# Performance work log

Measured on AMD Instinct MI355X. Metric: run time of the kernel, lower is better.

Reference implementation:

```python
import jax, jax.numpy as jnp
import numpy as np

B, N, D = 2, 2048, 1024
H, ENC = 16, 8
HD = D // H
EPS = 1e-5


def _apply_rope(x, cos, sin):
    # x: [B,N,H,HD], cos/sin: [N,HD//2]
    c = cos[None, :, None, :]
    s = sin[None, :, None, :]
    x_re = x[..., 0::2]
    x_im = x[..., 1::2]
    out = jnp.stack([x_re * c - x_im * s, x_re * s + x_im * c], axis=-1)
    return out.reshape(x.shape)


def _rmsnorm(x):
    return x * jax.lax.rsqrt(jnp.mean(x * x, axis=-1, keepdims=True) + EPS)


def setup_inputs() -> dict:
    key = jax.random.key(0)
    ks = jax.random.split(key, 8)
    pos = jnp.arange(N, dtype=jnp.float32)[:, None]
    inv_freq = 1.0 / (10000.0 ** (jnp.arange(0, HD, 2, dtype=jnp.float32) / HD))  # [HD//2]
    ang = pos * inv_freq[None, :]
    std = 0.02
    return {
        "x": jax.random.normal(ks[0], (B, N, D), dtype=jnp.float32),
        "rope_cos": jnp.cos(ang),
        "rope_sin": jnp.sin(ang),
        "Wq": std * jax.random.normal(ks[1], (D, D), dtype=jnp.float32),
        "Wk": std * jax.random.normal(ks[2], (D, D), dtype=jnp.float32),
        "Wv": std * jax.random.normal(ks[3], (D, D), dtype=jnp.float32),
        "Wo_enc": std * jax.random.normal(ks[4], (H * HD, D), dtype=jnp.float32),
        "Wo_dec": std * jax.random.normal(ks[5], ((H - ENC) * HD, D), dtype=jnp.float32),
        "heads": H,
        "encoder_heads": ENC,
    }


def reference(x, rope_cos, rope_sin, Wq, Wk, Wv, Wo_enc, Wo_dec, heads, encoder_heads):
    b, n, d = x.shape
    hd = d // heads
    scale = hd ** (-0.5)
    q = (x @ Wq).reshape(b, n, heads, hd)
    k = (x @ Wk).reshape(b, n, heads, hd)
    v = (x @ Wv).reshape(b, n, heads, hd)
    q = _rmsnorm(_apply_rope(q, rope_cos, rope_sin))
    k = _rmsnorm(_apply_rope(k, rope_cos, rope_sin))
    # scores: [B,H,N,N]
    scores = jnp.einsum("bihd,bjhd->bhij", q, k) * scale
    causal = jnp.tril(jnp.ones((n, n), dtype=bool))  # [N,N]
    is_enc = (jnp.arange(heads) < encoder_heads)[:, None, None]  # [H,1,1]
    allow = jnp.logical_or(is_enc, causal[None, :, :])  # [H,N,N]
    scores = jnp.where(allow[None], scores, -jnp.inf)
    att = jax.nn.softmax(scores, axis=-1)
    out = jnp.einsum("bhij,bjhd->bihd", att, v)  # [B,N,H,HD]
    enc_out = out.reshape(b, n, heads * hd) @ Wo_enc
    dec_out = out[:, :, encoder_heads:, :].reshape(b, n, (heads - encoder_heads) * hd) @ Wo_dec
    return (enc_out, dec_out)
```

## Files before the change

### kernel.cpp

```cpp
#include <hip/hip_runtime.h>
#include <hip/hip_bf16.h>
#include <math.h>

#define B_    2
#define N_    2048
#define D_    1024
#define H_    16
#define ENC_  8
#define HD_   64
#define EPS_  1e-5f
#define M_    (B_ * N_)

typedef __bf16 bf16x8 __attribute__((ext_vector_type(8)));
typedef __bf16 bf16x2 __attribute__((ext_vector_type(2)));
typedef float  f32x4  __attribute__((ext_vector_type(4)));

#define MB(x) ((size_t)(x) * 1024 * 1024)

#define KSC_  0.18033688011112042f

#if __has_builtin(__builtin_amdgcn_exp2f)
#define EXP2F(x) __builtin_amdgcn_exp2f(x)
#else
#define EXP2F(x) exp2f(x)
#endif

__device__ __forceinline__ void gld16(const __bf16* g, __bf16* l) {
    __builtin_amdgcn_global_load_lds(
        (const __attribute__((address_space(1))) void*)g,
        (__attribute__((address_space(3))) void*)l,
        16, 0, 0);
}

template <typename OutT>
__device__ __forceinline__ void gemm_core(
    const __bf16* __restrict__ A, const __bf16* __restrict__ Bt,
    OutT* __restrict__ C, int K, int lda, int aoff, int ldc,
    int bm, int bn, __bf16* As, __bf16* Bs)
{
    const int tid  = threadIdx.x;
    const int w    = tid >> 6;
    const int lane = tid & 63;
    const int lrow = lane & 15;
    const int quad = lane >> 4;
    const int wr   = w >> 1;
    const int wc   = w & 1;

    const int sr = lane >> 2;
    const int sc = (lane & 3) * 8;
    const __bf16* Ag0 = A  + (size_t)(bm +      w * 16 + sr) * lda + aoff + sc;
    const __bf16* Ag1 = A  + (size_t)(bm + 64 + w * 16 + sr) * lda + aoff + sc;
    const __bf16* Bg0 = Bt + (size_t)(bn +      w * 16 + sr) * K + sc;
    const __bf16* Bg1 = Bt + (size_t)(bn + 64 + w * 16 + sr) * K + sc;
    __bf16* Al0 = &As[w * 512];
    __bf16* Al1 = &As[2048 + w * 512];
    __bf16* Bl0 = &Bs[w * 512];
    __bf16* Bl1 = &Bs[2048 + w * 512];

    f32x4 acc[4][4];
    #pragma unroll
    for (int i = 0; i < 4; ++i)
        #pragma unroll
        for (int j = 0; j < 4; ++j) acc[i][j] = (f32x4){0.f, 0.f, 0.f, 0.f};

    for (int k0 = 0; k0 < K; k0 += 32) {
        gld16(Ag0 + k0, Al0);
        gld16(Ag1 + k0, Al1);
        gld16(Bg0 + k0, Bl0);
        gld16(Bg1 + k0, Bl1);
        __syncthreads();

        bf16x8 af[4], bf[4];
        #pragma unroll
        for (int rt = 0; rt < 4; ++rt)
            af[rt] = *(const bf16x8*)&As[(wr * 64 + rt * 16 + lrow) * 32 + quad * 8];
        #pragma unroll
        for (int ct = 0; ct < 4; ++ct)
            bf[ct] = *(const bf16x8*)&Bs[(wc * 64 + ct * 16 + lrow) * 32 + quad * 8];

        #pragma unroll
        for (int rt = 0; rt < 4; ++rt)
            #pragma unroll
            for (int ct = 0; ct < 4; ++ct)
                acc[rt][ct] = __builtin_amdgcn_mfma_f32_16x16x32_bf16(
                    af[rt], bf[ct], acc[rt][ct], 0, 0, 0);
        __syncthreads();
    }

    #pragma unroll
    for (int rt = 0; rt < 4; ++rt)
        #pragma unroll
        for (int ct = 0; ct < 4; ++ct)
            #pragma unroll
            for (int r = 0; r < 4; ++r) {
                const int row = bm + wr * 64 + rt * 16 + quad * 4 + r;
                const int col = bn + wc * 64 + ct * 16 + lrow;
                C[(size_t)row * ldc + col] = (OutT)acc[rt][ct][r];
            }
}

__global__ __launch_bounds__(256) void gemm_qkv(
    const __bf16* __restrict__ A, const __bf16* __restrict__ Bt,
    __bf16* __restrict__ C)
{
    __shared__ __bf16 As[128 * 32];
    __shared__ __bf16 Bs[128 * 32];
    gemm_core<__bf16>(A, Bt, C, D_, D_, 0, 3072,
                      blockIdx.y * 128, blockIdx.x * 128, As, Bs);
}

__global__ __launch_bounds__(256) void gemm_out(
    const __bf16* __restrict__ A, const __bf16* __restrict__ Woe,
    const __bf16* __restrict__ Wod, float* __restrict__ Cenc,
    float* __restrict__ Cdec)
{
    __shared__ __bf16 As[128 * 32];
    __shared__ __bf16 Bs[128 * 32];
    const int bx = blockIdx.x;
    if (bx < 8) {
        gemm_core<float>(A, Woe, Cenc, 1024, D_, 0, D_,
                         blockIdx.y * 128, bx * 128, As, Bs);
    } else {
        gemm_core<float>(A, Wod, Cdec, 512, D_, 512, D_,
                         blockIdx.y * 128, (bx - 8) * 128, As, Bs);
    }
}

struct WtArgs {
    const float* W[5];
    __bf16*      Wt[5];
    int          K[5];
    int          nyb[5];
    const float* x;
    __bf16*      xbf;
};

__global__ __launch_bounds__(256) void wt_conv_all(WtArgs ar)
{
    const int z = blockIdx.z;
    if (z >= 5) {
        const int linear = (z - 5) * 256 + blockIdx.y * 16 + blockIdx.x;
        const size_t i = ((size_t)linear * 256 + threadIdx.x) * 8;
        float4 a = *(const float4*)&ar.x[i];
        float4 b = *(const float4*)&ar.x[i + 4];
        bf16x8 o = {(__bf16)a.x, (__bf16)a.y, (__bf16)a.z, (__bf16)a.w,
                    (__bf16)b.x, (__bf16)b.y, (__bf16)b.z, (__bf16)b.w};
        *(bf16x8*)&ar.xbf[i] = o;
        return;
    }
    if (blockIdx.y >= ar.nyb[z]) return;
    const float* W  = ar.W[z];
    __bf16*      Wt = ar.Wt[z];
    const int    K  = ar.K[z];

    __shared__ __bf16 t[64][72];
    const int kb = blockIdx.y * 64;
    const int nb = blockIdx.x * 64;
    {
        const int kl = threadIdx.x >> 2;
        const int c0 = (threadIdx.x & 3) * 16;
        const float* src = W + (size_t)(kb + kl) * D_ + nb + c0;
        #pragma unroll
        for (int u = 0; u < 4; ++u) {
            float4 f = *(const float4*)&src[u * 4];
            t[c0 + u * 4 + 0][kl] = (__bf16)f.x;
            t[c0 + u * 4 + 1][kl] = (__bf16)f.y;
            t[c0 + u * 4 + 2][kl] = (__bf16)f.z;
            t[c0 + u * 4 + 3][kl] = (__bf16)f.w;
        }
    }
    __syncthreads();
    {
        const int nl  = threadIdx.x >> 2;
        const int k0c = (threadIdx.x & 3) * 16;
        __bf16* dst = Wt + (size_t)(nb + nl) * K + kb + k0c;
        *(bf16x8*)&dst[0] = *(const bf16x8*)&t[nl][k0c];
        *(bf16x8*)&dst[8] = *(const bf16x8*)&t[nl][k0c + 8];
    }
}

__global__ __launch_bounds__(256) void rope_vconv(
    const __bf16* __restrict__ qkv,
    const float* __restrict__ cs, const float* __restrict__ sn,
    __bf16* __restrict__ qbf, __bf16* __restrict__ kbf,
    __bf16* __restrict__ vt)
{
    if (blockIdx.x < 16384) {
        const int row  = blockIdx.x * 4 + (threadIdx.x >> 6);
        const int lane = threadIdx.x & 63;
        const int n    = (row >> 4) & (N_ - 1);
        const int b    = row >> 15;
        const int h    = row & 15;
        const int p    = lane >> 1;

        const float c = cs[n * (HD_ / 2) + p];
        const float s = sn[n * (HD_ / 2) + p];
        const size_t ibase = (size_t)(b * N_ + n) * 3072 + h * HD_ + lane;
        const size_t obase = ((size_t)(b * H_ + h) * N_ + n) * HD_ + lane;
        const bool odd = (lane & 1);

        {
            float val = (float)qkv[ibase];
            float partner = __shfl_xor(val, 1, 64);
            float r = odd ? fmaf(partner, s, val * c)
                          : (val * c - partner * s);
            float ss = r * r;
            #pragma unroll
            for (int off = 1; off < 64; off <<= 1) ss += __shfl_xor(ss, off, 64);
            qbf[obase] = (__bf16)(r * rsqrtf(ss * (1.0f / 64.0f) + EPS_) * KSC_);
        }
        {
            float val = (float)qkv[ibase + 1024];
            float partner = __shfl_xor(val, 1, 64);
            float r = odd ? fmaf(partner, s, val * c)
                          : (val * c - partner * s);
            float ss = r * r;
            #pragma unroll
            for (int off = 1; off < 64; off <<= 1) ss += __shfl_xor(ss, off, 64);
            kbf[obase] = (__bf16)(r * rsqrtf(ss * (1.0f / 64.0f) + EPS_));
        }
    } else {
        __shared__ __bf16 tile[64][72];
        const int bx = blockIdx.x - 16384;
        const int bh = bx >> 5;
        const int b  = bh >> 4, h = bh & 15;
        const int n0 = (bx & 31) * 64;
        {
            const int nl = threadIdx.x >> 2;
            const int d0 = (threadIdx.x & 3) * 16;
            const __bf16* src =
                qkv + (size_t)(b * N_ + n0 + nl) * 3072 + 2048 + h * HD_ + d0;
            bf16x8 v0 = *(const bf16x8*)&src[0];
            bf16x8 v1 = *(const bf16x8*)&src[8];
            #pragma unroll
            for (int e = 0; e < 8; ++e) {
                tile[d0 + e][nl]     = v0[e];
                tile[d0 + 8 + e][nl] = v1[e];
            }
        }
        __syncthreads();
        {
            const int dl = threadIdx.x >> 2;
            const int nc = (threadIdx.x & 3) * 16;
            __bf16* dst = vt + ((size_t)(bh * HD_ + dl)) * N_ + n0 + nc;
            bf16x8 o0, o1;
            #pragma unroll
            for (int e = 0; e < 8; ++e) {
                const int p0 = nc + e;
                const int p1 = nc + 8 + e;
                o0[e] = tile[dl][(p0 & ~31) + (((p0 >> 2) & 1) << 4)
                                 + (((p0 >> 3) & 3) << 2) + (p0 & 3)];
                o1[e] = tile[dl][(p1 & ~31) + (((p1 >> 2) & 1) << 4)
                                 + (((p1 >> 3) & 3) << 2) + (p1 & 3)];
            }
            *(bf16x8*)&dst[0] = o0;
            *(bf16x8*)&dst[8] = o1;
        }
    }
}

template <int NG, bool DEC>
__device__ __forceinline__ void attn_core(
    const __bf16* __restrict__ qbase, const __bf16* __restrict__ kbase,
    const __bf16* __restrict__ vbase, __bf16* __restrict__ o,
    int b, int h, int qb, int ntiles,
    __bf16 (*Ks)[4096], __bf16 (*Vs)[4096])
{
    const int tid  = threadIdx.x;
    const int w    = tid >> 6;
    const int lane = tid & 63;
    const int lrow = lane & 15;
    const int quad = lane >> 4;

    const __bf16* kg0 = kbase + (size_t)lane * HD_ + w * 8;
    const __bf16* kg1 = kbase + (size_t)lane * HD_ + (w + 4) * 8;
    const __bf16* vg  = vbase + (size_t)lane * N_;

    int i0g[NG];
    #pragma unroll
    for (int g = 0; g < NG; ++g) i0g[g] = qb * (NG * 64) + g * 64 + w * 16;

    bf16x8 qf[NG][2];
    #pragma unroll
    for (int g = 0; g < NG; ++g)
        #pragma unroll
        for (int kc = 0; kc < 2; ++kc)
            qf[g][kc] = *(const bf16x8*)
                &qbase[(size_t)(i0g[g] + lrow) * HD_ + kc * 32 + quad * 8];

    const f32x4 zero = {0.f, 0.f, 0.f, 0.f};
    f32x4 oacc[NG][4];
    float lsum[NG];
    #pragma unroll
    for (int g = 0; g < NG; ++g) {
        lsum[g] = 0.f;
        #pragma unroll
        for (int c = 0; c < 4; ++c) oacc[g][c] = zero;
    }

    auto stage = [&](int t, int bb) {
        const int j0 = t << 6;
        gld16(kg0 + (size_t)j0 * HD_, &Ks[bb][(w)     * 512]);
        gld16(kg1 + (size_t)j0 * HD_, &Ks[bb][(w + 4) * 512]);
        gld16(vg + j0 + w * 8,        &Vs[bb][(w)     * 512]);
        gld16(vg + j0 + (w + 4) * 8,  &Vs[bb][(w + 4) * 512]);
    };

    stage(0, 0);
    for (int t = 0; t < ntiles; ++t) {
        const int bb = t & 1;
        __syncthreads();
        if (t + 1 < ntiles) stage(t + 1, bb ^ 1);

        const int j64 = t << 6;
        const bool do1 = !DEC || (j64 + 32 <= i0g[0] + 15);

        bf16x8 pf[2][NG];

        {
            bf16x8 kf0 = *(const bf16x8*)&Ks[bb][((quad)     * 64 + lrow) * 8];
            bf16x8 kf1 = *(const bf16x8*)&Ks[bb][((4 + quad) * 64 + lrow) * 8];
            bf16x8 kf2 = *(const bf16x8*)&Ks[bb][((quad)     * 64 + 16 + lrow) * 8];
            bf16x8 kf3 = *(const bf16x8*)&Ks[bb][((4 + quad) * 64 + 16 + lrow) * 8];

            f32x4 s0[NG], s1[NG];
            #pragma unroll
            for (int g = 0; g < NG; ++g) { s0[g] = zero; s1[g] = zero; }
            #pragma unroll
            for (int g = 0; g < NG; ++g)
                s0[g] = __builtin_amdgcn_mfma_f32_16x16x32_bf16(kf0, qf[g][0], s0[g], 0, 0, 0);
            #pragma unroll
            for (int g = 0; g < NG; ++g)
                s0[g] = __builtin_amdgcn_mfma_f32_16x16x32_bf16(kf1, qf[g][1], s0[g], 0, 0, 0);
            #pragma unroll
            for (int g = 0; g < NG; ++g)
                s1[g] = __builtin_amdgcn_mfma_f32_16x16x32_bf16(kf2, qf[g][0], s1[g], 0, 0, 0);
            #pragma unroll
            for (int g = 0; g < NG; ++g)
                s1[g] = __builtin_amdgcn_mfma_f32_16x16x32_bf16(kf3, qf[g][1], s1[g], 0, 0, 0);

            #pragma unroll
            for (int g = 0; g < NG; ++g) {
                float pA[4], pB[4];
                if (DEC && (j64 + 31 > i0g[g])) {
                    const int i = i0g[g] + lrow;
                    #pragma unroll
                    for (int r = 0; r < 4; ++r) {
                        const int k0 = j64 + quad * 4 + r;
                        pA[r] = (k0      <= i) ? EXP2F(s0[g][r]) : 0.f;
                        pB[r] = (k0 + 16 <= i) ? EXP2F(s1[g][r]) : 0.f;
                    }
                } else {
                    #pragma unroll
                    for (int r = 0; r < 4; ++r) {
                        pA[r] = EXP2F(s0[g][r]);
                        pB[r] = EXP2F(s1[g][r]);
                    }
                }
                lsum[g] += (pA[0] + pA[1]) + (pA[2] + pA[3])
                         + (pB[0] + pB[1]) + (pB[2] + pB[3]);
                pf[0][g] = (bf16x8){(__bf16)pA[0], (__bf16)pA[1],
                                    (__bf16)pA[2], (__bf16)pA[3],
                                    (__bf16)pB[0], (__bf16)pB[1],
                                    (__bf16)pB[2], (__bf16)pB[3]};
            }
        }

        if (do1) {
            bf16x8 kf0 = *(const bf16x8*)&Ks[bb][((quad)     * 64 + 32 + lrow) * 8];
            bf16x8 kf1 = *(const bf16x8*)&Ks[bb][((4 + quad) * 64 + 32 + lrow) * 8];
            bf16x8 kf2 = *(const bf16x8*)&Ks[bb][((quad)     * 64 + 48 + lrow) * 8];
            bf16x8 kf3 = *(const bf16x8*)&Ks[bb][((4 + quad) * 64 + 48 + lrow) * 8];

            f32x4 s0[NG], s1[NG];
            #pragma unroll
            for (int g = 0; g < NG; ++g) { s0[g] = zero; s1[g] = zero; }
            #pragma unroll
            for (int g = 0; g < NG; ++g)
                s0[g] = __builtin_amdgcn_mfma_f32_16x16x32_bf16(kf0, qf[g][0], s0[g], 0, 0, 0);
            #pragma unroll
            for (int g = 0; g < NG; ++g)
                s0[g] = __builtin_amdgcn_mfma_f32_16x16x32_bf16(kf1, qf[g][1], s0[g], 0, 0, 0);
            #pragma unroll
            for (int g = 0; g < NG; ++g)
                s1[g] = __builtin_amdgcn_mfma_f32_16x16x32_bf16(kf2, qf[g][0], s1[g], 0, 0, 0);
            #pragma unroll
            for (int g = 0; g < NG; ++g)
                s1[g] = __builtin_amdgcn_mfma_f32_16x16x32_bf16(kf3, qf[g][1], s1[g], 0, 0, 0);

            const int jp = j64 + 32;
            #pragma unroll
            for (int g = 0; g < NG; ++g) {
                float pA[4], pB[4];
                if (DEC && (jp + 31 > i0g[g])) {
                    const int i = i0g[g] + lrow;
                    #pragma unroll
                    for (int r = 0; r < 4; ++r) {
                        const int k0 = jp + quad * 4 + r;
                        pA[r] = (k0      <= i) ? EXP2F(s0[g][r]) : 0.f;
                        pB[r] = (k0 + 16 <= i) ? EXP2F(s1[g][r]) : 0.f;
                    }
                } else {
                    #pragma unroll
                    for (int r = 0; r < 4; ++r) {
                        pA[r] = EXP2F(s0[g][r]);
                        pB[r] = EXP2F(s1[g][r]);
                    }
                }
                lsum[g] += (pA[0] + pA[1]) + (pA[2] + pA[3])
                         + (pB[0] + pB[1]) + (pB[2] + pB[3]);
                pf[1][g] = (bf16x8){(__bf16)pA[0], (__bf16)pA[1],
                                    (__bf16)pA[2], (__bf16)pA[3],
                                    (__bf16)pB[0], (__bf16)pB[1],
                                    (__bf16)pB[2], (__bf16)pB[3]};
            }
        }

        {
            bf16x8 vf0 = *(const bf16x8*)&Vs[bb][((quad) * 64 +  0 + lrow) * 8];
            bf16x8 vf1 = *(const bf16x8*)&Vs[bb][((quad) * 64 + 16 + lrow) * 8];
            bf16x8 vf2 = *(const bf16x8*)&Vs[bb][((quad) * 64 + 32 + lrow) * 8];
            bf16x8 vf3 = *(const bf16x8*)&Vs[bb][((quad) * 64 + 48 + lrow) * 8];
            #pragma unroll
            for (int g = 0; g < NG; ++g) {
                oacc[g][0] = __builtin_amdgcn_mfma_f32_16x16x32_bf16(pf[0][g], vf0, oacc[g][0], 0, 0, 0);
                oacc[g][1] = __builtin_amdgcn_mfma_f32_16x16x32_bf16(pf[0][g], vf1, oacc[g][1], 0, 0, 0);
                oacc[g][2] = __builtin_amdgcn_mfma_f32_16x16x32_bf16(pf[0][g], vf2, oacc[g][2], 0, 0, 0);
                oacc[g][3] = __builtin_amdgcn_mfma_f32_16x16x32_bf16(pf[0][g], vf3, oacc[g][3], 0, 0, 0);
            }
        }

        if (do1) {
            bf16x8 vf0 = *(const bf16x8*)&Vs[bb][((4 + quad) * 64 +  0 + lrow) * 8];
            bf16x8 vf1 = *(const bf16x8*)&Vs[bb][((4 + quad) * 64 + 16 + lrow) * 8];
            bf16x8 vf2 = *(const bf16x8*)&Vs[bb][((4 + quad) * 64 + 32 + lrow) * 8];
            bf16x8 vf3 = *(const bf16x8*)&Vs[bb][((4 + quad) * 64 + 48 + lrow) * 8];
            #pragma unroll
            for (int g = 0; g < NG; ++g) {
                oacc[g][0] = __builtin_amdgcn_mfma_f32_16x16x32_bf16(pf[1][g], vf0, oacc[g][0], 0, 0, 0);
                oacc[g][1] = __builtin_amdgcn_mfma_f32_16x16x32_bf16(pf[1][g], vf1, oacc[g][1], 0, 0, 0);
                oacc[g][2] = __builtin_amdgcn_mfma_f32_16x16x32_bf16(pf[1][g], vf2, oacc[g][2], 0, 0, 0);
                oacc[g][3] = __builtin_amdgcn_mfma_f32_16x16x32_bf16(pf[1][g], vf3, oacc[g][3], 0, 0, 0);
            }
        }
    }

    float lrec[NG][4];
    #pragma unroll
    for (int g = 0; g < NG; ++g) {
        float s = lsum[g];
        s += __shfl_xor(s, 16, 64);
        s += __shfl_xor(s, 32, 64);
        s = 1.0f / s;
        #pragma unroll
        for (int r = 0; r < 4; ++r)
            lrec[g][r] = __shfl(s, quad * 4 + r, 64);
    }

    #pragma unroll
    for (int g = 0; g < NG; ++g)
        #pragma unroll
        for (int c = 0; c < 4; ++c)
            #pragma unroll
            for (int r = 0; r < 4; ++r) {
                const int i = i0g[g] + quad * 4 + r;
                o[(size_t)(b * N_ + i) * D_ + h * HD_ + c * 16 + lrow] =
                    (__bf16)(oacc[g][c][r] * lrec[g][r]);
            }
}

__global__ __launch_bounds__(256) void attn_mfma(
    const __bf16* __restrict__ qbf, const __bf16* __restrict__ kbf,
    const __bf16* __restrict__ vtbf, __bf16* __restrict__ o)
{
    __shared__ __bf16 Ks[2][4096];
    __shared__ __bf16 Vs[2][4096];

    if (blockIdx.x < 256) {
        const int e  = blockIdx.x & 15;
        const int bh = (e >> 3) * 16 + (e & 7);
        const int qb = blockIdx.x >> 4;
        attn_core<2, false>(
            qbf  + (size_t)bh * N_ * HD_, kbf + (size_t)bh * N_ * HD_,
            vtbf + (size_t)bh * HD_ * N_, o,
            bh >> 4, bh & 15, qb, N_ >> 6, Ks, Vs);
    } else {
        const int idx = blockIdx.x - 256;
        const int d   = idx & 15;
        const int bh  = (d >> 3) * 16 + 8 + (d & 7);
        const int p   = idx >> 4;
        const int qb  = (p < 16) ? (31 - p) : (p - 16);
        attn_core<1, true>(
            qbf  + (size_t)bh * N_ * HD_, kbf + (size_t)bh * N_ * HD_,
            vtbf + (size_t)bh * HD_ * N_, o,
            bh >> 4, bh & 15, qb, qb + 1, Ks, Vs);
    }
}

extern "C" void kernel_launch(void* const* d_in, const int* in_sizes, int n_in,
                              void* d_out, int out_size, void* d_ws, size_t ws_size,
                              hipStream_t stream)
{
    const float* x   = (const float*)d_in[0];
    const float* cs  = (const float*)d_in[1];
    const float* sn  = (const float*)d_in[2];
    const float* Wq  = (const float*)d_in[3];
    const float* Wk  = (const float*)d_in[4];
    const float* Wv  = (const float*)d_in[5];
    const float* Woe = (const float*)d_in[6];
    const float* Wod = (const float*)d_in[7];

    float* enc_out = (float*)d_out;
    float* dec_out = enc_out + (size_t)M_ * D_;

    char* ws = (char*)d_ws;
    __bf16* xbf    = (__bf16*)(ws);
    __bf16* wqkv_t = (__bf16*)(ws + MB(8));
    __bf16* woe_t  = (__bf16*)(ws + MB(14));
    __bf16* wod_t  = (__bf16*)(ws + MB(16));
    __bf16* qkv    = (__bf16*)(ws + MB(17));
    __bf16* qbf    = (__bf16*)(ws + MB(41));
    __bf16* kbf    = (__bf16*)(ws + MB(49));
    __bf16* vtbf   = xbf;
    __bf16* obuf   = qkv;

    WtArgs wa;
    wa.W[0] = Wq;  wa.Wt[0] = wqkv_t;                 wa.K[0] = 1024; wa.nyb[0] = 16;
    wa.W[1] = Wk;  wa.Wt[1] = wqkv_t + 1024 * 1024;   wa.K[1] = 1024; wa.nyb[1] = 16;
    wa.W[2] = Wv;  wa.Wt[2] = wqkv_t + 2048 * 1024;   wa.K[2] = 1024; wa.nyb[2] = 16;
    wa.W[3] = Woe; wa.Wt[3] = woe_t;                  wa.K[3] = 1024; wa.nyb[3] = 16;
    wa.W[4] = Wod; wa.Wt[4] = wod_t;                  wa.K[4] = 512;  wa.nyb[4] = 8;
    wa.x = x; wa.xbf = xbf;
    wt_conv_all<<<dim3(16, 16, 13), 256, 0, stream>>>(wa);

    gemm_qkv<<<dim3(3072 / 128, M_ / 128), 256, 0, stream>>>(xbf, wqkv_t, qkv);

    rope_vconv<<<16384 + 1024, 256, 0, stream>>>(qkv, cs, sn, qbf, kbf, vtbf);

    attn_mfma<<<dim3(768), 256, 0, stream>>>(qbf, kbf, vtbf, obuf);

    gemm_out<<<dim3(16, M_ / 128), 256, 0, stream>>>(
        obuf, woe_t, wod_t, enc_out, dec_out);
}
```

Measured before the change: 222.3 us.

## Double GEMM K-tile to 64 with XOR-swizzled LDS and reorder output GEMM blocks

The shared GEMM core now stages a K-depth of 64 per iteration instead of 32, which halves the number of barrier pairs per GEMM. LDS rows are XOR-swizzled so the wider rows can be read without bank conflicts. The output-projection launch is flattened to a 1D grid that places all encoder-projection blocks before the decoder-projection blocks, changing scheduling order. LDS use per block doubles, which may lower occupancy.

```diff
diff --git a/kernel.cpp b/kernel.cpp
--- a/kernel.cpp
+++ b/kernel.cpp
@@ -46,16 +46,20 @@
     const int wr   = w >> 1;
     const int wc   = w & 1;
 
-    const int sr = lane >> 2;
-    const int sc = (lane & 3) * 8;
-    const __bf16* Ag0 = A  + (size_t)(bm +      w * 16 + sr) * lda + aoff + sc;
-    const __bf16* Ag1 = A  + (size_t)(bm + 64 + w * 16 + sr) * lda + aoff + sc;
-    const __bf16* Bg0 = Bt + (size_t)(bn +      w * 16 + sr) * K + sc;
-    const __bf16* Bg1 = Bt + (size_t)(bn + 64 + w * 16 + sr) * K + sc;
-    __bf16* Al0 = &As[w * 512];
-    __bf16* Al1 = &As[2048 + w * 512];
-    __bf16* Bl0 = &Bs[w * 512];
-    __bf16* Bl1 = &Bs[2048 + w * 512];
+    const int sr = lane >> 3;
+    const int cl = lane & 7;
+    const int sk = ((cl ^ sr) * 8);
+
+    const __bf16* Ag0 = A  + (size_t)(bm +  0 + w * 8 + sr) * lda + aoff + sk;
+    const __bf16* Ag1 = A  + (size_t)(bm + 32 + w * 8 + sr) * lda + aoff + sk;
+    const __bf16* Ag2 = A  + (size_t)(bm + 64 + w * 8 + sr) * lda + aoff + sk;
+    const __bf16* Ag3 = A  + (size_t)(bm + 96 + w * 8 + sr) * lda + aoff + sk;
+    const __bf16* Bg0 = Bt + (size_t)(bn +  0 + w * 8 + sr) * K + sk;
+    const __bf16* Bg1 = Bt + (size_t)(bn + 32 + w * 8 + sr) * K + sk;
+    const __bf16* Bg2 = Bt + (size_t)(bn + 64 + w * 8 + sr) * K + sk;
+    const __bf16* Bg3 = Bt + (size_t)(bn + 96 + w * 8 + sr) * K + sk;
+    __bf16* Al = As + w * 8 * 64;
+    __bf16* Bl = Bs + w * 8 * 64;
 
     f32x4 acc[4][4];
     #pragma unroll
@@ -63,27 +67,35 @@
         #pragma unroll
         for (int j = 0; j < 4; ++j) acc[i][j] = (f32x4){0.f, 0.f, 0.f, 0.f};
 
-    for (int k0 = 0; k0 < K; k0 += 32) {
-        gld16(Ag0 + k0, Al0);
-        gld16(Ag1 + k0, Al1);
-        gld16(Bg0 + k0, Bl0);
-        gld16(Bg1 + k0, Bl1);
+    for (int k0 = 0; k0 < K; k0 += 64) {
+        gld16(Ag0 + k0, Al);
+        gld16(Ag1 + k0, Al + 2048);
+        gld16(Ag2 + k0, Al + 4096);
+        gld16(Ag3 + k0, Al + 6144);
+        gld16(Bg0 + k0, Bl);
+        gld16(Bg1 + k0, Bl + 2048);
+        gld16(Bg2 + k0, Bl + 4096);
+        gld16(Bg3 + k0, Bl + 6144);
         __syncthreads();
 
-        bf16x8 af[4], bf[4];
-        #pragma unroll
-        for (int rt = 0; rt < 4; ++rt)
-            af[rt] = *(const bf16x8*)&As[(wr * 64 + rt * 16 + lrow) * 32 + quad * 8];
-        #pragma unroll
-        for (int ct = 0; ct < 4; ++ct)
-            bf[ct] = *(const bf16x8*)&Bs[(wc * 64 + ct * 16 + lrow) * 32 + quad * 8];
-
-        #pragma unroll
-        for (int rt = 0; rt < 4; ++rt)
+        #pragma unroll
+        for (int h = 0; h < 2; ++h) {
+            const int ch = ((h * 4 + quad) ^ (lrow & 7)) * 8;
+            bf16x8 af[4], bf[4];
+            #pragma unroll
+            for (int rt = 0; rt < 4; ++rt)
+                af[rt] = *(const bf16x8*)&As[(wr * 64 + rt * 16 + lrow) * 64 + ch];
             #pragma unroll
             for (int ct = 0; ct < 4; ++ct)
-                acc[rt][ct] = __builtin_amdgcn_mfma_f32_16x16x32_bf16(
-                    af[rt], bf[ct], acc[rt][ct], 0, 0, 0);
+                bf[ct] = *(const bf16x8*)&Bs[(wc * 64 + ct * 16 + lrow) * 64 + ch];
+
+            #pragma unroll
+            for (int rt = 0; rt < 4; ++rt)
+                #pragma unroll
+                for (int ct = 0; ct < 4; ++ct)
+                    acc[rt][ct] = __builtin_amdgcn_mfma_f32_16x16x32_bf16(
+                        af[rt], bf[ct], acc[rt][ct], 0, 0, 0);
+        }
         __syncthreads();
     }
 
@@ -103,8 +115,8 @@
     const __bf16* __restrict__ A, const __bf16* __restrict__ Bt,
     __bf16* __restrict__ C)
 {
-    __shared__ __bf16 As[128 * 32];
-    __shared__ __bf16 Bs[128 * 32];
+    __shared__ __bf16 As[128 * 64];
+    __shared__ __bf16 Bs[128 * 64];
     gemm_core<__bf16>(A, Bt, C, D_, D_, 0, 3072,
                       blockIdx.y * 128, blockIdx.x * 128, As, Bs);
 }
@@ -114,15 +126,16 @@
     const __bf16* __restrict__ Wod, float* __restrict__ Cenc,
     float* __restrict__ Cdec)
 {
-    __shared__ __bf16 As[128 * 32];
-    __shared__ __bf16 Bs[128 * 32];
-    const int bx = blockIdx.x;
-    if (bx < 8) {
+    __shared__ __bf16 As[128 * 64];
+    __shared__ __bf16 Bs[128 * 64];
+    const int id = blockIdx.x;
+    if (id < 256) {
         gemm_core<float>(A, Woe, Cenc, 1024, D_, 0, D_,
-                         blockIdx.y * 128, bx * 128, As, Bs);
+                         (id >> 3) * 128, (id & 7) * 128, As, Bs);
     } else {
+        const int idx = id - 256;
         gemm_core<float>(A, Wod, Cdec, 512, D_, 512, D_,
-                         blockIdx.y * 128, (bx - 8) * 128, As, Bs);
+                         (idx >> 3) * 128, (idx & 7) * 128, As, Bs);
     }
 }
 
@@ -539,6 +552,6 @@
 
     attn_mfma<<<dim3(768), 256, 0, stream>>>(qbf, kbf, vtbf, obuf);
 
-    gemm_out<<<dim3(16, M_ / 128), 256, 0, stream>>>(
+    gemm_out<<<dim3(512), 256, 0, stream>>>(
         obuf, woe_t, wod_t, enc_out, dec_out);
 }
```

Result: no change. 220.1 us (-1.0%).
